# Kernel optimization log

Hardware: AMD Instinct MI355X
Metric: run time of the kernel (lower is better)

The kernel has to match this reference:

```python
import jax, jax.numpy as jnp
import numpy as np

B, N, C, H = 8, 1024, 768, 12
HD = C // H
SCALE = HD ** -0.5
# iRPE 'product' config with ratio=1.9 (official get_rpe_config defaults)
ALPHA, BETA, GAMMA = 1.9, 3.8, 15.2
BETA_INT = int(BETA)          # 3
S = 2 * BETA_INT + 1          # 7 buckets per axis
NB = S * S                    # 49 buckets total


def _piecewise_index(d):
    # iRPE piecewise index: identity near zero, log-spaced further out, clipped at beta.
    d = d.astype(np.float64)
    ad = np.abs(d)
    far = np.sign(d) * np.clip(
        np.round(ALPHA + np.log(np.maximum(ad, 1e-6) / ALPHA) / np.log(GAMMA / ALPHA) * (BETA - ALPHA)),
        a_min=None, a_max=BETA)
    return np.where(ad <= ALPHA, np.round(d), far).astype(np.int64)


def _rp_bucket(n):
    # 2D 'product' relative-position buckets on a sqrt(n) x sqrt(n) grid.
    side = int(np.sqrt(n))
    ys, xs = np.divmod(np.arange(n), side)
    r = _piecewise_index(ys[:, None] - ys[None, :]) + BETA_INT  # [0, 2*beta_int]
    c = _piecewise_index(xs[:, None] - xs[None, :]) + BETA_INT
    return (r * S + c).astype(np.int32)  # [N, N] in [0, NB)


def setup_inputs() -> dict:
    key = jax.random.key(0)
    ks = jax.random.split(key, 8)
    q = jax.random.normal(ks[0], (B, N, C), jnp.float32)
    k = jax.random.normal(ks[1], (B, N, C), jnp.float32)
    v = jax.random.normal(ks[2], (B, N, C), jnp.float32)
    # shared-head contextual RPE tables
    w_rpe_q = jax.random.normal(ks[3], (HD, NB), jnp.float32) * 0.02
    w_rpe_k = jax.random.normal(ks[4], (HD, NB), jnp.float32) * 0.02
    w_rpe_v = jax.random.normal(ks[5], (NB, HD), jnp.float32) * 0.02
    proj_w = jax.random.normal(ks[6], (C, C), jnp.float32) * (C ** -0.5)
    proj_b = jax.random.normal(ks[7], (C,), jnp.float32) * 0.01
    rp_bucket = jnp.asarray(_rp_bucket(N))
    return dict(q=q, k=k, v=v, w_rpe_q=w_rpe_q, w_rpe_k=w_rpe_k,
                w_rpe_v=w_rpe_v, proj_w=proj_w, proj_b=proj_b, rp_bucket=rp_bucket)


def _gather_rows(t, rp_bucket):
    # t: [B,H,N,NB] -> bias[B,H,N,N]; bias[..., i, j] = t[..., i, rp_bucket[i, j]]
    rows = jnp.arange(t.shape[2])[:, None]
    return t[:, :, rows, rp_bucket]


def reference(q, k, v, w_rpe_q, w_rpe_k, w_rpe_v, proj_w, proj_b, rp_bucket):
    qh = q.reshape(B, N, H, HD).transpose(0, 2, 1, 3)  # [B,H,N,HD]
    kh = k.reshape(B, N, H, HD).transpose(0, 2, 1, 3)
    vh = v.reshape(B, N, H, HD).transpose(0, 2, 1, 3)
    attn = jnp.einsum('bhid,bhjd->bhij', qh, kh) * SCALE
    # rpe_k: q_i . W_k[:, bucket(i,j)]
    attn = attn + _gather_rows(jnp.einsum('bhid,du->bhiu', qh, w_rpe_k), rp_bucket)
    # rpe_q: (scale*k_j) . W_q[:, bucket(j,i)], then transposed onto (i,j)
    attn = attn + _gather_rows(jnp.einsum('bhjd,du->bhju', kh * SCALE, w_rpe_q), rp_bucket).swapaxes(2, 3)
    attn = jax.nn.softmax(attn, axis=-1)
    out = jnp.einsum('bhij,bhjd->bhid', attn, vh)
    # rpe_v: out_i += sum_j attn[i,j] * W_v[bucket(i,j)] via per-row bucket segment sums
    rows = jnp.arange(N)[:, None]
    bucket_sums = jnp.zeros((B, H, N, NB), attn.dtype).at[:, :, rows, rp_bucket].add(attn)
    out = out + jnp.einsum('bhiu,ud->bhid', bucket_sums, w_rpe_v)
    out = out.transpose(0, 2, 1, 3).reshape(B, N, C)
    out = out @ proj_w.T + proj_b
    return out, attn
```

## Files before the change

kernel.cpp:

```cpp
#include <hip/hip_runtime.h>

#define B_ 8
#define N_ 1024
#define C_ 768
#define H_ 12
#define HD_ 64
#define NB_ 49
#define BH_ 96
#define SCALE_ 0.125f

typedef unsigned int u32;
typedef unsigned short u16;
typedef __attribute__((ext_vector_type(8))) short mfrag;
typedef __attribute__((ext_vector_type(4))) float f32x4;
typedef __attribute__((ext_vector_type(4))) u32 u32x4;

__device__ __forceinline__ u16 f2bf(float x) {
    u32 u = __float_as_uint(x);
    u32 r = u + 0x7FFFu + ((u >> 16) & 1u);
    return (u16)(r >> 16);
}
__device__ __forceinline__ float bf2f(u16 h) { return __uint_as_float(((u32)h) << 16); }

__device__ __forceinline__ int lutf(int d) {
    int a = d < 0 ? -d : d;
    int gg = (a < 2 ? a : 2) + (a >= 4 ? 1 : 0);
    return d < 0 ? 3 - gg : 3 + gg;
}

__global__ void irpe_prep_k(const float* __restrict__ q, const float* __restrict__ k,
                            const float* __restrict__ w_rpe_q, const float* __restrict__ w_rpe_k,
                            u16* __restrict__ qh, u16* __restrict__ ql,
                            u16* __restrict__ kh, u16* __restrict__ kl,
                            float* __restrict__ tk, u16* __restrict__ tqT) {
    const int bh = blockIdx.y, b = bh / H_, h = bh % H_;
    const int row0 = blockIdx.x * 4;
    __shared__ float qs[4][HD_], ks[4][HD_];
    const int t = threadIdx.x;
    {
        const int r = t >> 6, d = t & 63;
        const size_t gi = ((size_t)(b * N_ + row0 + r)) * C_ + h * HD_ + d;
        const float vq = q[gi], vk = k[gi];
        qs[r][d] = vq;
        ks[r][d] = vk;
        const size_t so = (((size_t)(bh << 10)) + row0 + r) * 64 + d;
        const u16 qhi = f2bf(vq), khi = f2bf(vk);
        qh[so] = qhi; ql[so] = f2bf(vq - bf2f(qhi));
        kh[so] = khi; kl[so] = f2bf(vk - bf2f(khi));
    }
    __syncthreads();
    if (t < 4 * NB_) {
        const int r = t / NB_, u = t - r * NB_;
        float dk = 0.f, dq = 0.f;
#pragma unroll
        for (int d = 0; d < HD_; ++d) {
            dk = fmaf(qs[r][d], w_rpe_k[d * NB_ + u], dk);
            dq = fmaf(ks[r][d], w_rpe_q[d * NB_ + u], dq);
        }
        tk[((size_t)bh * N_ + row0 + r) * NB_ + u] = dk;
        tqT[(((size_t)bh * NB_ + u) << 10) + row0 + r] = f2bf(dq * SCALE_);
    }
}

__global__ void irpe_vt_k(const float* __restrict__ v, u16* __restrict__ vth) {
    __shared__ float tile[64][65];
    const int bh = blockIdx.y, jc0 = blockIdx.x * 64;
    const int b = bh / H_, h = bh % H_;
    const int t = threadIdx.x;
#pragma unroll
    for (int rep = 0; rep < 4; ++rep) {
        const int fl = rep * 256 + t;
        const int jr = fl >> 4, c4 = (fl & 15) * 4;
        const float4 x = *(const float4*)&v[((size_t)(b * N_ + jc0 + jr)) * C_ + h * HD_ + c4];
        tile[jr][c4] = x.x; tile[jr][c4 + 1] = x.y; tile[jr][c4 + 2] = x.z; tile[jr][c4 + 3] = x.w;
    }
    __syncthreads();
    const int d = t >> 2, jq = (t & 3) * 16;
    u32 ph[8];
#pragma unroll
    for (int jj = 0; jj < 8; ++jj) {
        const u16 h0 = f2bf(tile[jq + jj * 2][d]);
        const u16 h1 = f2bf(tile[jq + jj * 2 + 1][d]);
        ph[jj] = (u32)h0 | ((u32)h1 << 16);
    }
    const size_t dst = (((size_t)bh * 64 + d) << 10) + jc0 + jq;
    *(uint4*)&vth[dst] = make_uint4(ph[0], ph[1], ph[2], ph[3]);
    *(uint4*)&vth[dst + 8] = make_uint4(ph[4], ph[5], ph[6], ph[7]);
}

__global__ __launch_bounds__(256, 3) void irpe_attn_mfma_k(
    const u16* __restrict__ qh_g, const u16* __restrict__ ql_g,
    const u16* __restrict__ kh_g, const u16* __restrict__ kl_g,
    const u16* __restrict__ vth_g,
    const float* __restrict__ tk, const u16* __restrict__ tqT,
    u16* __restrict__ e_g, float* __restrict__ s_arr, float* __restrict__ pre) {
    __shared__ u16 kAh[4096], kAl[4096];
    __shared__ u16 vAh[4096];
    __shared__ u16 awh[4096];
    __shared__ u16 tq_su[NB_ * 72];
    __shared__ u16 tks_s[64 * 50];

    const int gid = blockIdx.x;
    const int xcd = gid & 7, L = gid >> 3;
    const int bh = xcd * 12 + (L >> 4);
    const int itile = L & 15;
    const int b = bh / H_, h = bh % H_;
    const int i0 = itile * 64;
    const int t = threadIdx.x;
    const int w = t >> 6, lane = t & 63;
    const int ln4 = lane >> 4, lh15 = lane & 15;
    const int yi = itile * 2 + (w >> 1);
    const size_t tqbase = (size_t)bh * NB_ * 1024;
    const int arow0 = (bh << 10) + i0;

    mfrag qAh[2], qAl[2];
#pragma unroll
    for (int ks = 0; ks < 2; ++ks) {
        const size_t qa = (((size_t)(bh << 10) + i0 + w * 16 + lh15) << 6) + (ln4 << 3) + (ks << 5);
        qAh[ks] = *(const mfrag*)&qh_g[qa];
        qAl[ks] = *(const mfrag*)&ql_g[qa];
    }

    int bxp[2][4];
#pragma unroll
    for (int jh = 0; jh < 2; ++jh)
#pragma unroll
        for (int r = 0; r < 4; ++r) {
            const int xi = (w & 1) * 16 + ln4 * 4 + r;
            bxp[jh][r] = lutf(xi - (jh * 16 + lh15));
        }

    mfrag kstg[4], vstg[2];
#pragma unroll
    for (int rep = 0; rep < 2; ++rep) {
        const int unit = rep * 256 + t;
        const int row = unit >> 3, un = unit & 7;
        const size_t ka = (((size_t)(bh << 10) + row) << 6) + un * 8;
        kstg[rep * 2] = *(const mfrag*)&kh_g[ka];
        kstg[rep * 2 + 1] = *(const mfrag*)&kl_g[ka];
        vstg[rep] = *(const mfrag*)&vth_g[(((size_t)(bh * 64) + row) << 10) + un * 8];
    }
    u32x4 tqpre[2];
    {
        const int u0 = t >> 3, c0 = t & 7;
        tqpre[0] = *(const u32x4*)&tqT[tqbase + ((size_t)u0 << 10) + c0 * 8];
        if (t < 136) {
            const int u1 = (256 + t) >> 3, c1 = t & 7;
            tqpre[1] = *(const u32x4*)&tqT[tqbase + ((size_t)u1 << 10) + c1 * 8];
        }
    }

    {
        const size_t tkb = ((size_t)(bh << 10) + i0) * NB_;
        for (int idx = t; idx < 64 * NB_; idx += 256) {
            const int row = idx / NB_, u = idx - row * NB_;
            tks_s[row * 50 + u] = f2bf(tk[tkb + idx]);
        }
    }

    f32x4 apv[4] = {{0.f, 0.f, 0.f, 0.f}, {0.f, 0.f, 0.f, 0.f},
                    {0.f, 0.f, 0.f, 0.f}, {0.f, 0.f, 0.f, 0.f}};
    float srow[4] = {0.f, 0.f, 0.f, 0.f};

#pragma unroll 1
    for (int ch = 0; ch < 16; ++ch) {
        const int jc0 = ch << 6;

#pragma unroll
        for (int rep = 0; rep < 2; ++rep) {
            const int unit = rep * 256 + t;
            const int row = unit >> 3, un = unit & 7;
            const int ldso = row * 128 + ((un ^ (row & 7)) << 4);
            *(mfrag*)((char*)kAh + ldso) = kstg[rep * 2];
            *(mfrag*)((char*)kAl + ldso) = kstg[rep * 2 + 1];
            *(mfrag*)((char*)vAh + ldso) = vstg[rep];
        }
        {
            const int u0 = t >> 3, c0 = t & 7;
            *(u32x4*)((char*)tq_su + u0 * 144 + c0 * 16) = tqpre[0];
            if (t < 136) {
                const int u1 = (256 + t) >> 3;
                *(u32x4*)((char*)tq_su + u1 * 144 + (t & 7) * 16) = tqpre[1];
            }
        }
        __syncthreads();

        f32x4 aq[4];
        __builtin_amdgcn_s_setprio(1);
#pragma unroll
        for (int ji = 0; ji < 4; ++ji) {
            const int rb = ji * 16 + lh15, swb = rb & 7;
            const mfrag bh0 = *(const mfrag*)((const char*)kAh + rb * 128 + ((ln4 ^ swb) << 4));
            const mfrag bl0 = *(const mfrag*)((const char*)kAl + rb * 128 + ((ln4 ^ swb) << 4));
            const mfrag bh1 = *(const mfrag*)((const char*)kAh + rb * 128 + (((4 + ln4) ^ swb) << 4));
            const mfrag bl1 = *(const mfrag*)((const char*)kAl + rb * 128 + (((4 + ln4) ^ swb) << 4));
            f32x4 c = {0.f, 0.f, 0.f, 0.f};
            c = __builtin_amdgcn_mfma_f32_16x16x32_bf16(qAh[0], bh0, c, 0, 0, 0);
            c = __builtin_amdgcn_mfma_f32_16x16x32_bf16(qAh[0], bl0, c, 0, 0, 0);
            c = __builtin_amdgcn_mfma_f32_16x16x32_bf16(qAl[0], bh0, c, 0, 0, 0);
            c = __builtin_amdgcn_mfma_f32_16x16x32_bf16(qAh[1], bh1, c, 0, 0, 0);
            c = __builtin_amdgcn_mfma_f32_16x16x32_bf16(qAh[1], bl1, c, 0, 0, 0);
            c = __builtin_amdgcn_mfma_f32_16x16x32_bf16(qAl[1], bh1, c, 0, 0, 0);
            aq[ji] = c;
        }
        __builtin_amdgcn_s_setprio(0);

        if (ch < 15) {
            const int jc1 = jc0 + 64;
#pragma unroll
            for (int rep = 0; rep < 2; ++rep) {
                const int unit = rep * 256 + t;
                const int row = unit >> 3, un = unit & 7;
                const size_t ka = (((size_t)(bh << 10) + jc1 + row) << 6) + un * 8;
                kstg[rep * 2] = *(const mfrag*)&kh_g[ka];
                kstg[rep * 2 + 1] = *(const mfrag*)&kl_g[ka];
                vstg[rep] = *(const mfrag*)&vth_g[(((size_t)(bh * 64) + row) << 10) + jc1 + un * 8];
            }
            const int u0 = t >> 3, c0 = t & 7;
            tqpre[0] = *(const u32x4*)&tqT[tqbase + ((size_t)u0 << 10) + jc1 + c0 * 8];
            if (t < 136) {
                const int u1 = (256 + t) >> 3;
                tqpre[1] = *(const u32x4*)&tqT[tqbase + ((size_t)u1 << 10) + jc1 + (t & 7) * 8];
            }
        }

#pragma unroll
        for (int ji = 0; ji < 4; ++ji) {
            const int yj = (ch << 1) + (ji >> 1);
            const int by7 = 7 * lutf(yi - yj);
            const int jl = ji * 16 + lh15;
#pragma unroll
            for (int r = 0; r < 4; ++r) {
                const int il = w * 16 + ln4 * 4 + r;
                const int bij = by7 + bxp[ji & 1][r];
                const float e = __expf(fmaf(aq[ji][r], SCALE_,
                                            bf2f(tks_s[il * 50 + bij]) + bf2f(tq_su[(48 - bij) * 72 + jl])));
                srow[r] += e;
                const int off = il * 128 + ((jl << 1) ^ ((il & 7) << 4));
                *(u16*)((char*)awh + off) = f2bf(e);
            }
        }

        {
            const int rowA = w * 16 + lh15, sa = (rowA & 7) << 4;
            mfrag pah[2];
#pragma unroll
            for (int ks = 0; ks < 2; ++ks)
                pah[ks] = *(const mfrag*)((const char*)awh + rowA * 128 + ((((ln4 << 4) + (ks << 6))) ^ sa));
            __builtin_amdgcn_s_setprio(1);
#pragma unroll
            for (int di = 0; di < 4; ++di) {
                const int rv = di * 16 + lh15, swv = rv & 7;
                const mfrag vh0 = *(const mfrag*)((const char*)vAh + rv * 128 + ((ln4 ^ swv) << 4));
                const mfrag vh1 = *(const mfrag*)((const char*)vAh + rv * 128 + (((4 + ln4) ^ swv) << 4));
                f32x4 c = apv[di];
                c = __builtin_amdgcn_mfma_f32_16x16x32_bf16(pah[0], vh0, c, 0, 0, 0);
                c = __builtin_amdgcn_mfma_f32_16x16x32_bf16(pah[1], vh1, c, 0, 0, 0);
                apv[di] = c;
            }
            __builtin_amdgcn_s_setprio(0);
        }

#pragma unroll
        for (int rep = 0; rep < 2; ++rep) {
            const int unit = rep * 64 + lane;
            const int rowl = unit >> 3, un = unit & 7;
            const int row = w * 16 + rowl;
            const u32x4 val = *(const u32x4*)((const char*)awh + row * 128 + ((un << 4) ^ ((row & 7) << 4)));
            __builtin_nontemporal_store(val,
                (u32x4*)&e_g[((size_t)(arow0 + row) << 11) + jc0 + un * 8]);
        }
        __syncthreads();
    }

    float inv[4];
#pragma unroll
    for (int r = 0; r < 4; ++r) {
        float s = srow[r];
        s += __shfl_xor(s, 1); s += __shfl_xor(s, 2);
        s += __shfl_xor(s, 4); s += __shfl_xor(s, 8);
        inv[r] = 1.0f / s;
        if (lh15 == 0) s_arr[((size_t)bh << 10) + i0 + w * 16 + ln4 * 4 + r] = s;
    }

#pragma unroll
    for (int di = 0; di < 4; ++di) {
        const int d = di * 16 + lh15;
#pragma unroll
        for (int r = 0; r < 4; ++r) {
            const int i = i0 + w * 16 + ln4 * 4 + r;
            pre[((size_t)(b * N_ + i)) * C_ + h * HD_ + d] = apv[di][r] * inv[r];
        }
    }
}

__global__ __launch_bounds__(256) void irpe_rescale_bucket_k(
    float* __restrict__ attn, const float* __restrict__ s_arr, float* __restrict__ bs) {
    __shared__ float R[8][32][8];
    __shared__ float inv_s[8];
    __shared__ int lutyj[32];

    const int gid = blockIdx.x;
    const int xcd = gid & 7, loc = gid >> 3;
    const int bh = xcd * 12 + (loc >> 7);
    const int i0 = (loc & 127) * 8;
    const int t = threadIdx.x;
    const int w = t >> 6, lane = t & 63;
    const int yi2 = i0 >> 5;

    for (int idx = t; idx < 8 * 32 * 8; idx += 256) ((float*)R)[idx] = 0.f;
    if (t < 8) inv_s[t] = 1.0f / s_arr[((size_t)bh << 10) + i0 + t];
    if (t < 32) lutyj[t] = lutf(yi2 - t);
    __syncthreads();

    const int j0 = lane * 16;
    const int yj = j0 >> 5;
    const int xb = j0 & 31;

#pragma unroll
    for (int rp = 0; rp < 2; ++rp) {
        const int rr = rp * 4 + w;
        const int i = i0 + rr;
        const int xi = i & 31;
        const float inv = inv_s[rr];
        const u16* erow = (const u16*)attn + (((size_t)((bh << 10) + i)) << 11);
        const u32x4 ea = *(const u32x4*)&erow[j0];
        const u32x4 eb = *(const u32x4*)&erow[j0 + 8];
        float ev[16];
        {
            const u32 wds[8] = {ea.x, ea.y, ea.z, ea.w, eb.x, eb.y, eb.z, eb.w};
#pragma unroll
            for (int m = 0; m < 8; ++m) {
                ev[2 * m] = bf2f((u16)(wds[m] & 0xFFFFu));
                ev[2 * m + 1] = bf2f((u16)(wds[m] >> 16));
            }
        }

        float acc = 0.f;
        int cur = lutf(xi - xb);
#pragma unroll
        for (int c = 0; c < 16; ++c) {
            const int bx_ = lutf(xi - (xb + c));
            if (bx_ != cur) { atomicAdd(&R[rr][yj][cur], acc); acc = 0.f; cur = bx_; }
            acc += ev[c];
        }
        atomicAdd(&R[rr][yj][cur], acc);

        float* rowf = &attn[((size_t)((bh << 10) + i)) << 10];
#pragma unroll
        for (int m = 0; m < 4; ++m) {
            const f32x4 o = {ev[4 * m] * inv, ev[4 * m + 1] * inv,
                             ev[4 * m + 2] * inv, ev[4 * m + 3] * inv};
            *(f32x4*)&rowf[j0 + 4 * m] = o;
        }
    }
    __syncthreads();

    for (int idx = t; idx < 8 * NB_; idx += 256) {
        const int rr = idx / NB_, u = idx - rr * NB_;
        const int by = u / 7, bx = u - by * 7;
        float s = 0.f;
#pragma unroll
        for (int yj2 = 0; yj2 < 32; ++yj2)
            if (lutyj[yj2] == by) s += R[rr][yj2][bx];
        bs[((size_t)((bh << 10) + i0 + rr)) * NB_ + u] = s * inv_s[rr];
    }
}

__global__ void irpe_addpre_k(const float* __restrict__ bs, const float* __restrict__ w_rpe_v,
                              float* __restrict__ pre) {
    __shared__ float wv[NB_ * 64];
    __shared__ float bss[16 * 52];
    const int bh = blockIdx.y, b = bh / H_, h = bh % H_;
    const int i0 = blockIdx.x * 16;
    const int t = threadIdx.x;
    for (int idx = t; idx < NB_ * 64; idx += 256) wv[idx] = w_rpe_v[idx];
    for (int idx = t; idx < 16 * NB_; idx += 256) {
        const int il = idx / NB_, u = idx - il * NB_;
        bss[il * 52 + u] = bs[((size_t)((bh << 10) + i0 + il)) * NB_ + u];
    }
    __syncthreads();
    const int il = t >> 4, d4 = (t & 15) * 4;
    f32x4 acc = {0.f, 0.f, 0.f, 0.f};
    for (int u = 0; u < NB_; ++u) {
        const float bv = bss[il * 52 + u];
        const f32x4 wvv = *(const f32x4*)&wv[u * 64 + d4];
        acc += bv * wvv;
    }
    float* p = &pre[((size_t)(b * N_ + i0 + il)) * C_ + h * HD_ + d4];
    f32x4 old = *(const f32x4*)p;
    *(f32x4*)p = old + acc;
}

__global__ __launch_bounds__(256, 4) void irpe_proj_mfma_k(
    const float* __restrict__ A, const float* __restrict__ Bw,
    const float* __restrict__ bias, float* __restrict__ Cout) {
    __shared__ u16 Ah[4096], Al[4096], Bh[4096], Bl[4096];
    const int bm = blockIdx.x * 64, bn = blockIdx.y * 64;
    const int t = threadIdx.x;
    const int w = t >> 6, lane = t & 63;
    const int ln4 = lane >> 4, lh15 = lane & 15;

    f32x4 acc[4] = {{0.f, 0.f, 0.f, 0.f}, {0.f, 0.f, 0.f, 0.f},
                    {0.f, 0.f, 0.f, 0.f}, {0.f, 0.f, 0.f, 0.f}};
    float bias_r[4];
#pragma unroll
    for (int ji = 0; ji < 4; ++ji) bias_r[ji] = bias[bn + ji * 16 + lh15];

    const int srow_ = t >> 3, sun = t & 7;
    const int ldso = srow_ * 128 + ((sun ^ (srow_ & 7)) << 4);

    for (int kt = 0; kt < C_; kt += 64) {
#pragma unroll
        for (int rep = 0; rep < 2; ++rep) {
            const int row = rep * 32 + srow_;
            const int ldo = ldso + rep * 32 * 128;
            const float* ap = &A[(size_t)(bm + row) * C_ + kt + sun * 8];
            const float* bp = &Bw[(size_t)(bn + row) * C_ + kt + sun * 8];
            const float4 a0 = *(const float4*)ap, a1 = *(const float4*)(ap + 4);
            const float4 b0 = *(const float4*)bp, b1 = *(const float4*)(bp + 4);
            const float av[8] = {a0.x, a0.y, a0.z, a0.w, a1.x, a1.y, a1.z, a1.w};
            const float bv[8] = {b0.x, b0.y, b0.z, b0.w, b1.x, b1.y, b1.z, b1.w};
            u32 ahh[4], all_[4], bhh[4], bll[4];
#pragma unroll
            for (int jj = 0; jj < 4; ++jj) {
                const u16 h0 = f2bf(av[jj * 2]), h1 = f2bf(av[jj * 2 + 1]);
                ahh[jj] = (u32)h0 | ((u32)h1 << 16);
                all_[jj] = (u32)f2bf(av[jj * 2] - bf2f(h0)) | ((u32)f2bf(av[jj * 2 + 1] - bf2f(h1)) << 16);
                const u16 g0 = f2bf(bv[jj * 2]), g1 = f2bf(bv[jj * 2 + 1]);
                bhh[jj] = (u32)g0 | ((u32)g1 << 16);
                bll[jj] = (u32)f2bf(bv[jj * 2] - bf2f(g0)) | ((u32)f2bf(bv[jj * 2 + 1] - bf2f(g1)) << 16);
            }
            *(uint4*)((char*)Ah + ldo) = make_uint4(ahh[0], ahh[1], ahh[2], ahh[3]);
            *(uint4*)((char*)Al + ldo) = make_uint4(all_[0], all_[1], all_[2], all_[3]);
            *(uint4*)((char*)Bh + ldo) = make_uint4(bhh[0], bhh[1], bhh[2], bhh[3]);
            *(uint4*)((char*)Bl + ldo) = make_uint4(bll[0], bll[1], bll[2], bll[3]);
        }
        __syncthreads();

        const int ra = w * 16 + lh15, sa = ra & 7;
        const mfrag aF0h = *(const mfrag*)((const char*)Ah + ra * 128 + ((ln4 ^ sa) << 4));
        const mfrag aF0l = *(const mfrag*)((const char*)Al + ra * 128 + ((ln4 ^ sa) << 4));
        const mfrag aF1h = *(const mfrag*)((const char*)Ah + ra * 128 + (((4 + ln4) ^ sa) << 4));
        const mfrag aF1l = *(const mfrag*)((const char*)Al + ra * 128 + (((4 + ln4) ^ sa) << 4));
#pragma unroll
        for (int ji = 0; ji < 4; ++ji) {
            const int rb = ji * 16 + lh15, sb = rb & 7;
            const mfrag bF0h = *(const mfrag*)((const char*)Bh + rb * 128 + ((ln4 ^ sb) << 4));
            const mfrag bF0l = *(const mfrag*)((const char*)Bl + rb * 128 + ((ln4 ^ sb) << 4));
            const mfrag bF1h = *(const mfrag*)((const char*)Bh + rb * 128 + (((4 + ln4) ^ sb) << 4));
            const mfrag bF1l = *(const mfrag*)((const char*)Bl + rb * 128 + (((4 + ln4) ^ sb) << 4));
            f32x4 c = acc[ji];
            c = __builtin_amdgcn_mfma_f32_16x16x32_bf16(aF0h, bF0h, c, 0, 0, 0);
            c = __builtin_amdgcn_mfma_f32_16x16x32_bf16(aF0h, bF0l, c, 0, 0, 0);
            c = __builtin_amdgcn_mfma_f32_16x16x32_bf16(aF0l, bF0h, c, 0, 0, 0);
            c = __builtin_amdgcn_mfma_f32_16x16x32_bf16(aF1h, bF1h, c, 0, 0, 0);
            c = __builtin_amdgcn_mfma_f32_16x16x32_bf16(aF1h, bF1l, c, 0, 0, 0);
            c = __builtin_amdgcn_mfma_f32_16x16x32_bf16(aF1l, bF1h, c, 0, 0, 0);
            acc[ji] = c;
        }
        __syncthreads();
    }

#pragma unroll
    for (int ji = 0; ji < 4; ++ji) {
        const int col = bn + ji * 16 + lh15;
#pragma unroll
        for (int r = 0; r < 4; ++r) {
            const int row = bm + w * 16 + ln4 * 4 + r;
            Cout[(size_t)row * C_ + col] = acc[ji][r] + bias_r[ji];
        }
    }
}

extern "C" void kernel_launch(void* const* d_in, const int* in_sizes, int n_in,
                              void* d_out, int out_size, void* d_ws, size_t ws_size,
                              hipStream_t stream) {
    const float* q       = (const float*)d_in[0];
    const float* k       = (const float*)d_in[1];
    const float* v       = (const float*)d_in[2];
    const float* w_rpe_q = (const float*)d_in[3];
    const float* w_rpe_k = (const float*)d_in[4];
    const float* w_rpe_v = (const float*)d_in[5];
    const float* proj_w  = (const float*)d_in[6];
    const float* proj_b  = (const float*)d_in[7];

    float* out  = (float*)d_out;
    float* attn = out + (size_t)B_ * N_ * C_;

    char* ws = (char*)d_ws;
    float* tk    = (float*)ws; ws += (size_t)BH_ * N_ * NB_ * 4;
    u16*   tqT   = (u16*)ws;   ws += (size_t)BH_ * NB_ * N_ * 2;
    float* pre   = (float*)ws; ws += (size_t)B_ * N_ * C_ * 4;
    float* s_arr = (float*)ws; ws += (size_t)BH_ * N_ * 4;
    float* bs    = (float*)ws; ws += (size_t)BH_ * N_ * NB_ * 4;
    u16* qh  = (u16*)ws; ws += (size_t)BH_ * N_ * 64 * 2;
    u16* ql  = (u16*)ws; ws += (size_t)BH_ * N_ * 64 * 2;
    u16* kh  = (u16*)ws; ws += (size_t)BH_ * N_ * 64 * 2;
    u16* kl  = (u16*)ws; ws += (size_t)BH_ * N_ * 64 * 2;
    u16* vth = (u16*)ws; ws += (size_t)BH_ * 64 * N_ * 2;

    irpe_prep_k<<<dim3(N_ / 4, BH_), 256, 0, stream>>>(q, k, w_rpe_q, w_rpe_k,
                                                       qh, ql, kh, kl, tk, tqT);
    irpe_vt_k<<<dim3(16, BH_), 256, 0, stream>>>(v, vth);

    irpe_attn_mfma_k<<<BH_ * (N_ / 64), 256, 0, stream>>>(
        qh, ql, kh, kl, vth, tk, tqT, (u16*)attn, s_arr, pre);

    irpe_rescale_bucket_k<<<BH_ * (N_ / 8), 256, 0, stream>>>(attn, s_arr, bs);
    irpe_addpre_k<<<dim3(N_ / 16, BH_), 256, 0, stream>>>(bs, w_rpe_v, pre);
    irpe_proj_mfma_k<<<dim3((B_ * N_) / 64, C_ / 64), 256, 0, stream>>>(pre, proj_w, proj_b, out);
}
```

Measured before the change: 565.4 us.

## Fuse softmax rescale and bucket segment sums into attention kernel epilogue

The separate rescale/bucket kernel is removed. Its work now runs as an 8-pass epilogue inside the attention kernel. Row sums stay in shared memory rather than a global s_arr buffer, and the bf16 scores are re-read right after being written, now with regular instead of nontemporal stores so they are likely still in cache. This saves a kernel launch and a global round trip of the sums, at the cost of a longer serial tail per attention block that reuses kAh shared memory as the bucket accumulator.

```diff
diff --git a/kernel.cpp b/kernel.cpp
--- a/kernel.cpp
+++ b/kernel.cpp
@@ -93,12 +93,15 @@
     const u16* __restrict__ kh_g, const u16* __restrict__ kl_g,
     const u16* __restrict__ vth_g,
     const float* __restrict__ tk, const u16* __restrict__ tqT,
-    u16* __restrict__ e_g, float* __restrict__ s_arr, float* __restrict__ pre) {
+    u16* __restrict__ e_g, float* __restrict__ attn_f,
+    float* __restrict__ bs, float* __restrict__ pre) {
     __shared__ u16 kAh[4096], kAl[4096];
     __shared__ u16 vAh[4096];
     __shared__ u16 awh[4096];
     __shared__ u16 tq_su[NB_ * 72];
     __shared__ u16 tks_s[64 * 50];
+    __shared__ float ssum_s[64];
+    __shared__ int lutyj_s[32];
 
     const int gid = blockIdx.x;
     const int xcd = gid & 7, L = gid >> 3;
@@ -267,8 +270,7 @@
             const int rowl = unit >> 3, un = unit & 7;
             const int row = w * 16 + rowl;
             const u32x4 val = *(const u32x4*)((const char*)awh + row * 128 + ((un << 4) ^ ((row & 7) << 4)));
-            __builtin_nontemporal_store(val,
-                (u32x4*)&e_g[((size_t)(arow0 + row) << 11) + jc0 + un * 8]);
+            *(u32x4*)&e_g[((size_t)(arow0 + row) << 11) + jc0 + un * 8] = val;
         }
         __syncthreads();
     }
@@ -280,7 +282,7 @@
         s += __shfl_xor(s, 1); s += __shfl_xor(s, 2);
         s += __shfl_xor(s, 4); s += __shfl_xor(s, 8);
         inv[r] = 1.0f / s;
-        if (lh15 == 0) s_arr[((size_t)bh << 10) + i0 + w * 16 + ln4 * 4 + r] = s;
+        if (lh15 == 0) ssum_s[w * 16 + ln4 * 4 + r] = s;
     }
 
 #pragma unroll
@@ -292,78 +294,68 @@
             pre[((size_t)(b * N_ + i)) * C_ + h * HD_ + d] = apv[di][r] * inv[r];
         }
     }
-}
-
-__global__ __launch_bounds__(256) void irpe_rescale_bucket_k(
-    float* __restrict__ attn, const float* __restrict__ s_arr, float* __restrict__ bs) {
-    __shared__ float R[8][32][8];
-    __shared__ float inv_s[8];
-    __shared__ int lutyj[32];
-
-    const int gid = blockIdx.x;
-    const int xcd = gid & 7, loc = gid >> 3;
-    const int bh = xcd * 12 + (loc >> 7);
-    const int i0 = (loc & 127) * 8;
-    const int t = threadIdx.x;
-    const int w = t >> 6, lane = t & 63;
-    const int yi2 = i0 >> 5;
-
-    for (int idx = t; idx < 8 * 32 * 8; idx += 256) ((float*)R)[idx] = 0.f;
-    if (t < 8) inv_s[t] = 1.0f / s_arr[((size_t)bh << 10) + i0 + t];
-    if (t < 32) lutyj[t] = lutf(yi2 - t);
-    __syncthreads();
-
+
+    float* Rbuf = (float*)kAh;
     const int j0 = lane * 16;
-    const int yj = j0 >> 5;
-    const int xb = j0 & 31;
-
-#pragma unroll
-    for (int rp = 0; rp < 2; ++rp) {
-        const int rr = rp * 4 + w;
-        const int i = i0 + rr;
-        const int xi = i & 31;
-        const float inv = inv_s[rr];
-        const u16* erow = (const u16*)attn + (((size_t)((bh << 10) + i)) << 11);
-        const u32x4 ea = *(const u32x4*)&erow[j0];
-        const u32x4 eb = *(const u32x4*)&erow[j0 + 8];
-        float ev[16];
-        {
-            const u32 wds[8] = {ea.x, ea.y, ea.z, ea.w, eb.x, eb.y, eb.z, eb.w};
-#pragma unroll
-            for (int m = 0; m < 8; ++m) {
-                ev[2 * m] = bf2f((u16)(wds[m] & 0xFFFFu));
-                ev[2 * m + 1] = bf2f((u16)(wds[m] >> 16));
-            }
-        }
-
-        float acc = 0.f;
-        int cur = lutf(xi - xb);
-#pragma unroll
-        for (int c = 0; c < 16; ++c) {
-            const int bx_ = lutf(xi - (xb + c));
-            if (bx_ != cur) { atomicAdd(&R[rr][yj][cur], acc); acc = 0.f; cur = bx_; }
-            acc += ev[c];
-        }
-        atomicAdd(&R[rr][yj][cur], acc);
-
-        float* rowf = &attn[((size_t)((bh << 10) + i)) << 10];
-#pragma unroll
-        for (int m = 0; m < 4; ++m) {
-            const f32x4 o = {ev[4 * m] * inv, ev[4 * m + 1] * inv,
-                             ev[4 * m + 2] * inv, ev[4 * m + 3] * inv};
-            *(f32x4*)&rowf[j0 + 4 * m] = o;
-        }
-    }
-    __syncthreads();
-
-    for (int idx = t; idx < 8 * NB_; idx += 256) {
-        const int rr = idx / NB_, u = idx - rr * NB_;
-        const int by = u / 7, bx = u - by * 7;
-        float s = 0.f;
-#pragma unroll
-        for (int yj2 = 0; yj2 < 32; ++yj2)
-            if (lutyj[yj2] == by) s += R[rr][yj2][bx];
-        bs[((size_t)((bh << 10) + i0 + rr)) * NB_ + u] = s * inv_s[rr];
+    const int yj = j0 >> 5, xb = j0 & 31;
+
+#pragma unroll 1
+    for (int p = 0; p < 8; ++p) {
+        for (int idx = t; idx < 2048; idx += 256) Rbuf[idx] = 0.f;
+        if (t < 32) lutyj_s[t] = lutf((((i0 + p * 8) >> 5)) - t);
+        __syncthreads();
+
+#pragma unroll
+        for (int rp = 0; rp < 2; ++rp) {
+            const int rr = rp * 4 + w;
+            const int lr = p * 8 + rr;
+            const int i = i0 + lr;
+            const int xi = i & 31;
+            const float invv = 1.0f / ssum_s[lr];
+            const u16* erow = e_g + ((size_t)(arow0 + lr) << 11);
+            const u32x4 ea = *(const u32x4*)&erow[j0];
+            const u32x4 eb = *(const u32x4*)&erow[j0 + 8];
+            float ev[16];
+            {
+                const u32 wds[8] = {ea.x, ea.y, ea.z, ea.w, eb.x, eb.y, eb.z, eb.w};
+#pragma unroll
+                for (int m = 0; m < 8; ++m) {
+                    ev[2 * m] = bf2f((u16)(wds[m] & 0xFFFFu));
+                    ev[2 * m + 1] = bf2f((u16)(wds[m] >> 16));
+                }
+            }
+
+            float acc = 0.f;
+            int cur = lutf(xi - xb);
+#pragma unroll
+            for (int c = 0; c < 16; ++c) {
+                const int bx_ = lutf(xi - (xb + c));
+                if (bx_ != cur) { atomicAdd(&Rbuf[(rr * 32 + yj) * 8 + cur], acc); acc = 0.f; cur = bx_; }
+                acc += ev[c];
+            }
+            atomicAdd(&Rbuf[(rr * 32 + yj) * 8 + cur], acc);
+
+            float* rowf = &attn_f[(size_t)(arow0 + lr) << 10];
+#pragma unroll
+            for (int m = 0; m < 4; ++m) {
+                const f32x4 o = {ev[4 * m] * invv, ev[4 * m + 1] * invv,
+                                 ev[4 * m + 2] * invv, ev[4 * m + 3] * invv};
+                *(f32x4*)&rowf[j0 + 4 * m] = o;
+            }
+        }
+        __syncthreads();
+
+        for (int idx = t; idx < 8 * NB_; idx += 256) {
+            const int rr = idx / NB_, u = idx - rr * NB_;
+            const int by = u / 7, bx = u - by * 7;
+            float s = 0.f;
+#pragma unroll
+            for (int yj2 = 0; yj2 < 32; ++yj2)
+                if (lutyj_s[yj2] == by) s += Rbuf[(rr * 32 + yj2) * 8 + bx];
+            const int lr = p * 8 + rr;
+            bs[((size_t)(arow0 + lr)) * NB_ + u] = s / ssum_s[lr];
+        }
+        __syncthreads();
     }
 }
 
@@ -492,7 +484,6 @@
     float* tk    = (float*)ws; ws += (size_t)BH_ * N_ * NB_ * 4;
     u16*   tqT   = (u16*)ws;   ws += (size_t)BH_ * NB_ * N_ * 2;
     float* pre   = (float*)ws; ws += (size_t)B_ * N_ * C_ * 4;
-    float* s_arr = (float*)ws; ws += (size_t)BH_ * N_ * 4;
     float* bs    = (float*)ws; ws += (size_t)BH_ * N_ * NB_ * 4;
     u16* qh  = (u16*)ws; ws += (size_t)BH_ * N_ * 64 * 2;
     u16* ql  = (u16*)ws; ws += (size_t)BH_ * N_ * 64 * 2;
@@ -505,9 +496,8 @@
     irpe_vt_k<<<dim3(16, BH_), 256, 0, stream>>>(v, vth);
 
     irpe_attn_mfma_k<<<BH_ * (N_ / 64), 256, 0, stream>>>(
-        qh, ql, kh, kl, vth, tk, tqT, (u16*)attn, s_arr, pre);
-
-    irpe_rescale_bucket_k<<<BH_ * (N_ / 8), 256, 0, stream>>>(attn, s_arr, bs);
+        qh, ql, kh, kl, vth, tk, tqT, (u16*)attn, attn, bs, pre);
+
     irpe_addpre_k<<<dim3(N_ / 16, BH_), 256, 0, stream>>>(bs, w_rpe_v, pre);
     irpe_proj_mfma_k<<<dim3((B_ * N_) / 64, C_ / 64), 256, 0, stream>>>(pre, proj_w, proj_b, out);
 }
```

After: 605.0 us. 1.07x slower.

## Fuse bucket-sum into rescale kernel and pre-split proj operands to bf16 hi/lo

Applied to the files above, without the earlier changes.

Folds the separate addpre kernel into the rescale/bucket kernel, so the bucket sums stay in shared memory and are multiplied by W_v there. The same kernel writes the pre-projection activations directly as bf16 hi/lo pairs. The projection weight is split once by a new small kernel, so the projection GEMM loads ready bf16 tiles instead of converting fp32 in every block, and its MFMA loop is wrapped in setprio. The cost is loading W_v (12.5 KB) into shared memory in each of the 12288 rescale blocks, which may lower occupancy and add redundant traffic.

```diff
diff --git a/kernel.cpp b/kernel.cpp
--- a/kernel.cpp
+++ b/kernel.cpp
@@ -62,6 +62,16 @@
     }
 }
 
+__global__ void irpe_prep_w_k(const float* __restrict__ W,
+                              u16* __restrict__ wh, u16* __restrict__ wl) {
+    const int o = (blockIdx.x * 256 + threadIdx.x) * 4;
+    const float4 x = *(const float4*)&W[o];
+    const u16 h0 = f2bf(x.x), h1 = f2bf(x.y), h2 = f2bf(x.z), h3 = f2bf(x.w);
+    *(ushort4*)&wh[o] = make_ushort4(h0, h1, h2, h3);
+    *(ushort4*)&wl[o] = make_ushort4(f2bf(x.x - bf2f(h0)), f2bf(x.y - bf2f(h1)),
+                                     f2bf(x.z - bf2f(h2)), f2bf(x.w - bf2f(h3)));
+}
+
 __global__ void irpe_vt_k(const float* __restrict__ v, u16* __restrict__ vth) {
     __shared__ float tile[64][65];
     const int bh = blockIdx.y, jc0 = blockIdx.x * 64;
@@ -294,9 +304,13 @@
     }
 }
 
-__global__ __launch_bounds__(256) void irpe_rescale_bucket_k(
-    float* __restrict__ attn, const float* __restrict__ s_arr, float* __restrict__ bs) {
+__global__ __launch_bounds__(256) void irpe_rescale_fuse_k(
+    float* __restrict__ attn, const float* __restrict__ s_arr,
+    const float* __restrict__ pre, const float* __restrict__ w_rpe_v,
+    u16* __restrict__ preh, u16* __restrict__ prel) {
     __shared__ float R[8][32][8];
+    __shared__ float wv[NB_ * 64];
+    __shared__ float bss[8][52];
     __shared__ float inv_s[8];
     __shared__ int lutyj[32];
 
@@ -304,11 +318,13 @@
     const int xcd = gid & 7, loc = gid >> 3;
     const int bh = xcd * 12 + (loc >> 7);
     const int i0 = (loc & 127) * 8;
+    const int b = bh / H_, h = bh % H_;
     const int t = threadIdx.x;
     const int w = t >> 6, lane = t & 63;
     const int yi2 = i0 >> 5;
 
     for (int idx = t; idx < 8 * 32 * 8; idx += 256) ((float*)R)[idx] = 0.f;
+    for (int idx = t; idx < NB_ * 64; idx += 256) wv[idx] = w_rpe_v[idx];
     if (t < 8) inv_s[t] = 1.0f / s_arr[((size_t)bh << 10) + i0 + t];
     if (t < 32) lutyj[t] = lutf(yi2 - t);
     __syncthreads();
@@ -363,37 +379,24 @@
 #pragma unroll
         for (int yj2 = 0; yj2 < 32; ++yj2)
             if (lutyj[yj2] == by) s += R[rr][yj2][bx];
-        bs[((size_t)((bh << 10) + i0 + rr)) * NB_ + u] = s * inv_s[rr];
-    }
-}
-
-__global__ void irpe_addpre_k(const float* __restrict__ bs, const float* __restrict__ w_rpe_v,
-                              float* __restrict__ pre) {
-    __shared__ float wv[NB_ * 64];
-    __shared__ float bss[16 * 52];
-    const int bh = blockIdx.y, b = bh / H_, h = bh % H_;
-    const int i0 = blockIdx.x * 16;
-    const int t = threadIdx.x;
-    for (int idx = t; idx < NB_ * 64; idx += 256) wv[idx] = w_rpe_v[idx];
-    for (int idx = t; idx < 16 * NB_; idx += 256) {
-        const int il = idx / NB_, u = idx - il * NB_;
-        bss[il * 52 + u] = bs[((size_t)((bh << 10) + i0 + il)) * NB_ + u];
+        bss[rr][u] = s * inv_s[rr];
     }
     __syncthreads();
-    const int il = t >> 4, d4 = (t & 15) * 4;
-    f32x4 acc = {0.f, 0.f, 0.f, 0.f};
-    for (int u = 0; u < NB_; ++u) {
-        const float bv = bss[il * 52 + u];
-        const f32x4 wvv = *(const f32x4*)&wv[u * 64 + d4];
-        acc += bv * wvv;
-    }
-    float* p = &pre[((size_t)(b * N_ + i0 + il)) * C_ + h * HD_ + d4];
-    f32x4 old = *(const f32x4*)p;
-    *(f32x4*)p = old + acc;
+
+    for (int idx = t; idx < 512; idx += 256) {
+        const int rr = idx >> 6, d = idx & 63;
+        const size_t row = (size_t)(b * N_ + i0 + rr);
+        float acc = pre[row * C_ + h * HD_ + d];
+        for (int u = 0; u < NB_; ++u) acc = fmaf(bss[rr][u], wv[u * 64 + d], acc);
+        const u16 hi = f2bf(acc);
+        preh[row * C_ + h * HD_ + d] = hi;
+        prel[row * C_ + h * HD_ + d] = f2bf(acc - bf2f(hi));
+    }
 }
 
 __global__ __launch_bounds__(256, 4) void irpe_proj_mfma_k(
-    const float* __restrict__ A, const float* __restrict__ Bw,
+    const u16* __restrict__ Ah_g, const u16* __restrict__ Al_g,
+    const u16* __restrict__ Bh_g, const u16* __restrict__ Bl_g,
     const float* __restrict__ bias, float* __restrict__ Cout) {
     __shared__ u16 Ah[4096], Al[4096], Bh[4096], Bl[4096];
     const int bm = blockIdx.x * 64, bn = blockIdx.y * 64;
@@ -415,26 +418,12 @@
         for (int rep = 0; rep < 2; ++rep) {
             const int row = rep * 32 + srow_;
             const int ldo = ldso + rep * 32 * 128;
-            const float* ap = &A[(size_t)(bm + row) * C_ + kt + sun * 8];
-            const float* bp = &Bw[(size_t)(bn + row) * C_ + kt + sun * 8];
-            const float4 a0 = *(const float4*)ap, a1 = *(const float4*)(ap + 4);
-            const float4 b0 = *(const float4*)bp, b1 = *(const float4*)(bp + 4);
-            const float av[8] = {a0.x, a0.y, a0.z, a0.w, a1.x, a1.y, a1.z, a1.w};
-            const float bv[8] = {b0.x, b0.y, b0.z, b0.w, b1.x, b1.y, b1.z, b1.w};
-            u32 ahh[4], all_[4], bhh[4], bll[4];
-#pragma unroll
-            for (int jj = 0; jj < 4; ++jj) {
-                const u16 h0 = f2bf(av[jj * 2]), h1 = f2bf(av[jj * 2 + 1]);
-                ahh[jj] = (u32)h0 | ((u32)h1 << 16);
-                all_[jj] = (u32)f2bf(av[jj * 2] - bf2f(h0)) | ((u32)f2bf(av[jj * 2 + 1] - bf2f(h1)) << 16);
-                const u16 g0 = f2bf(bv[jj * 2]), g1 = f2bf(bv[jj * 2 + 1]);
-                bhh[jj] = (u32)g0 | ((u32)g1 << 16);
-                bll[jj] = (u32)f2bf(bv[jj * 2] - bf2f(g0)) | ((u32)f2bf(bv[jj * 2 + 1] - bf2f(g1)) << 16);
-            }
-            *(uint4*)((char*)Ah + ldo) = make_uint4(ahh[0], ahh[1], ahh[2], ahh[3]);
-            *(uint4*)((char*)Al + ldo) = make_uint4(all_[0], all_[1], all_[2], all_[3]);
-            *(uint4*)((char*)Bh + ldo) = make_uint4(bhh[0], bhh[1], bhh[2], bhh[3]);
-            *(uint4*)((char*)Bl + ldo) = make_uint4(bll[0], bll[1], bll[2], bll[3]);
+            const size_t ao = (size_t)(bm + row) * C_ + kt + sun * 8;
+            const size_t bo = (size_t)(bn + row) * C_ + kt + sun * 8;
+            *(u32x4*)((char*)Ah + ldo) = *(const u32x4*)&Ah_g[ao];
+            *(u32x4*)((char*)Al + ldo) = *(const u32x4*)&Al_g[ao];
+            *(u32x4*)((char*)Bh + ldo) = *(const u32x4*)&Bh_g[bo];
+            *(u32x4*)((char*)Bl + ldo) = *(const u32x4*)&Bl_g[bo];
         }
         __syncthreads();
 
@@ -443,6 +432,7 @@
         const mfrag aF0l = *(const mfrag*)((const char*)Al + ra * 128 + ((ln4 ^ sa) << 4));
         const mfrag aF1h = *(const mfrag*)((const char*)Ah + ra * 128 + (((4 + ln4) ^ sa) << 4));
         const mfrag aF1l = *(const mfrag*)((const char*)Al + ra * 128 + (((4 + ln4) ^ sa) << 4));
+        __builtin_amdgcn_s_setprio(1);
 #pragma unroll
         for (int ji = 0; ji < 4; ++ji) {
             const int rb = ji * 16 + lh15, sb = rb & 7;
@@ -459,6 +449,7 @@
             c = __builtin_amdgcn_mfma_f32_16x16x32_bf16(aF1l, bF1h, c, 0, 0, 0);
             acc[ji] = c;
         }
+        __builtin_amdgcn_s_setprio(0);
         __syncthreads();
     }
 
@@ -493,21 +484,26 @@
     u16*   tqT   = (u16*)ws;   ws += (size_t)BH_ * NB_ * N_ * 2;
     float* pre   = (float*)ws; ws += (size_t)B_ * N_ * C_ * 4;
     float* s_arr = (float*)ws; ws += (size_t)BH_ * N_ * 4;
-    float* bs    = (float*)ws; ws += (size_t)BH_ * N_ * NB_ * 4;
-    u16* qh  = (u16*)ws; ws += (size_t)BH_ * N_ * 64 * 2;
-    u16* ql  = (u16*)ws; ws += (size_t)BH_ * N_ * 64 * 2;
-    u16* kh  = (u16*)ws; ws += (size_t)BH_ * N_ * 64 * 2;
-    u16* kl  = (u16*)ws; ws += (size_t)BH_ * N_ * 64 * 2;
-    u16* vth = (u16*)ws; ws += (size_t)BH_ * 64 * N_ * 2;
+    u16* qh   = (u16*)ws; ws += (size_t)BH_ * N_ * 64 * 2;
+    u16* ql   = (u16*)ws; ws += (size_t)BH_ * N_ * 64 * 2;
+    u16* kh   = (u16*)ws; ws += (size_t)BH_ * N_ * 64 * 2;
+    u16* kl   = (u16*)ws; ws += (size_t)BH_ * N_ * 64 * 2;
+    u16* vth  = (u16*)ws; ws += (size_t)BH_ * 64 * N_ * 2;
+    u16* preh = (u16*)ws; ws += (size_t)B_ * N_ * C_ * 2;
+    u16* prel = (u16*)ws; ws += (size_t)B_ * N_ * C_ * 2;
+    u16* wh   = (u16*)ws; ws += (size_t)C_ * C_ * 2;
+    u16* wl   = (u16*)ws; ws += (size_t)C_ * C_ * 2;
 
     irpe_prep_k<<<dim3(N_ / 4, BH_), 256, 0, stream>>>(q, k, w_rpe_q, w_rpe_k,
                                                        qh, ql, kh, kl, tk, tqT);
+    irpe_prep_w_k<<<(C_ * C_) / 1024, 256, 0, stream>>>(proj_w, wh, wl);
     irpe_vt_k<<<dim3(16, BH_), 256, 0, stream>>>(v, vth);
 
     irpe_attn_mfma_k<<<BH_ * (N_ / 64), 256, 0, stream>>>(
         qh, ql, kh, kl, vth, tk, tqT, (u16*)attn, s_arr, pre);
 
-    irpe_rescale_bucket_k<<<BH_ * (N_ / 8), 256, 0, stream>>>(attn, s_arr, bs);
-    irpe_addpre_k<<<dim3(N_ / 16, BH_), 256, 0, stream>>>(bs, w_rpe_v, pre);
-    irpe_proj_mfma_k<<<dim3((B_ * N_) / 64, C_ / 64), 256, 0, stream>>>(pre, proj_w, proj_b, out);
-}
+    irpe_rescale_fuse_k<<<BH_ * (N_ / 8), 256, 0, stream>>>(attn, s_arr, pre,
+                                                            w_rpe_v, preh, prel);
+    irpe_proj_mfma_k<<<dim3((B_ * N_) / 64, C_ / 64), 256, 0, stream>>>(
+        preh, prel, wh, wl, proj_b, out);
+}
```

Result: no change. 565.5 us (+0.0%).
